# Kernel optimization log

Measured on AMD Instinct MI355X. Metric: run time of the kernel, lower is better.

## Reference

```python
import jax, jax.numpy as jnp
import numpy as np

N_NODES = 100000
N_EDGES = 1600000
IN_FEATS = 256
OUT_FEATS = 128


def setup_inputs() -> dict:
    key = jax.random.key(0)
    k1, k2, k3, k4 = jax.random.split(key, 4)
    feat = jax.random.normal(k1, (N_NODES, IN_FEATS), dtype=jnp.float32)
    W = jax.random.normal(k2, (IN_FEATS, OUT_FEATS), dtype=jnp.float32)
    src = jax.random.randint(k3, (N_EDGES,), 0, N_NODES, dtype=jnp.int64)
    dst = jax.random.randint(k4, (N_EDGES,), 0, N_NODES, dtype=jnp.int64)
    return {"feat": feat, "W": W, "src": src, "dst": dst}


def reference(feat, W, src, dst):
    # h_self = feat @ W  -> [N, out_feats]
    h_self = feat @ W
    # update_all(copy_src('h','m'), sum('m','neigh')): gather source features,
    # scatter-sum at destination nodes (SpMM over the edge list).
    msgs = h_self[src]                                        # [E, out_feats]
    h_neigh = jax.ops.segment_sum(msgs, dst, num_segments=N_NODES)
    # in-degree per node
    degs = jax.ops.segment_sum(jnp.ones(dst.shape, jnp.float32), dst,
                               num_segments=N_NODES)          # [N]
    rst = (h_neigh + h_self) / (degs[:, None] + 1.0)
    return jax.nn.relu(rst)
```

## Files before the change

kernel.cpp:

```cpp
#include <hip/hip_runtime.h>
#include <hip/hip_bf16.h>


#define IN_FEATS 256
#define OUT_FEATS 128
#define NUM_NODES 100000
#define NUM_EDGES 1600000

#define NB 782
#define EC 128
#define CHUNK_E 12500
#define BCAP 3072
#define GEMM_BLOCKS 391

typedef __attribute__((ext_vector_type(8))) short short8;
typedef __attribute__((ext_vector_type(8))) unsigned short ushort8;
typedef __attribute__((ext_vector_type(4))) float f32x4;

static __device__ inline unsigned short f2bfu(float x) {
    union { __hip_bfloat16 h; unsigned short u; } c;
    c.h = __float2bfloat16(x);
    return c.u;
}
static __device__ inline ushort2 f2bfu2(float x, float y) {
    union { __hip_bfloat162 h; ushort2 u; } c;
    c.h = __float22bfloat162_rn(make_float2(x, y));
    return c.u;
}
static __device__ inline float bf2f(unsigned short h) {
    return __uint_as_float((unsigned)h << 16);
}

__global__ __launch_bounds__(256) void convert_hist(
    const float* __restrict__ W, unsigned short* __restrict__ Wt,
    const int* __restrict__ dst, int* __restrict__ counts)
{
    int b = blockIdx.x;
    int t = threadIdx.x;
    if (b < 128) {
        int i = b * 256 + t;
        int n = i >> 8;
        int k = i & 255;
        Wt[i] = f2bfu(W[(size_t)k * OUT_FEATS + n]);
        return;
    }
    int c = b - 128;
    __shared__ int hist[NB];
    for (int i = t; i < NB; i += 256) hist[i] = 0;
    __syncthreads();
    const int4* dp = (const int4*)(dst + c * CHUNK_E);
    for (int i = t; i < CHUNK_E / 4; i += 256) {
        int4 d4 = dp[i];
        atomicAdd(&hist[d4.x >> 7], 1);
        atomicAdd(&hist[d4.y >> 7], 1);
        atomicAdd(&hist[d4.z >> 7], 1);
        atomicAdd(&hist[d4.w >> 7], 1);
    }
    __syncthreads();
    for (int i = t; i < NB; i += 256) counts[c * NB + i] = hist[i];
}

__global__ __launch_bounds__(128) void scan_chunks(
    int* __restrict__ counts, int* __restrict__ bucket_total)
{
    __shared__ int sd[128];
    int b = blockIdx.x, t = threadIdx.x;
    int v = counts[t * NB + b];
    sd[t] = v;
    __syncthreads();
    for (int o = 1; o < 128; o <<= 1) {
        int x = (t >= o) ? sd[t - o] : 0;
        __syncthreads();
        sd[t] += x;
        __syncthreads();
    }
    counts[t * NB + b] = sd[t] - v;
    if (t == 127) bucket_total[b] = sd[127];
}

__global__ __launch_bounds__(256) void scan_buckets(
    const int* __restrict__ bucket_total, int* __restrict__ bucket_base)
{
    __shared__ int sd[256];
    int t = threadIdx.x;
    int base = t * 4;
    int v0 = 0, v1 = 0, v2 = 0, v3 = 0;
    if (base + 3 < NB) {
        int4 v = *(const int4*)&bucket_total[base];
        v0 = v.x; v1 = v.y; v2 = v.z; v3 = v.w;
    } else {
        if (base + 0 < NB) v0 = bucket_total[base + 0];
        if (base + 1 < NB) v1 = bucket_total[base + 1];
        if (base + 2 < NB) v2 = bucket_total[base + 2];
        if (base + 3 < NB) v3 = bucket_total[base + 3];
    }
    int s = v0 + v1 + v2 + v3;
    sd[t] = s;
    __syncthreads();
    for (int o = 1; o < 256; o <<= 1) {
        int x = (t >= o) ? sd[t - o] : 0;
        __syncthreads();
        sd[t] += x;
        __syncthreads();
    }
    int e0 = sd[t] - s, e1 = e0 + v0, e2 = e1 + v1, e3 = e2 + v2;
    if (base + 0 < NB) bucket_base[base + 0] = e0;
    if (base + 1 < NB) bucket_base[base + 1] = e1;
    if (base + 2 < NB) bucket_base[base + 2] = e2;
    if (base + 3 < NB) bucket_base[base + 3] = e3;
}

__global__ __launch_bounds__(512) void scatter_k(
    const int* __restrict__ src, const int* __restrict__ dst,
    const int* __restrict__ counts, const int* __restrict__ bucket_base,
    int* __restrict__ bedges)
{
    __shared__ int cur[NB];
    const int tid = threadIdx.x;
    int c = blockIdx.x;
    for (int i = tid; i < NB; i += 512)
        cur[i] = bucket_base[i] + counts[c * NB + i];
    __syncthreads();
    const int4* dp = (const int4*)(dst + c * CHUNK_E);
    const int4* sp = (const int4*)(src + c * CHUNK_E);
    for (int i = tid; i < CHUNK_E / 4; i += 512) {
        int4 d4 = dp[i];
        int4 s4 = sp[i];
        int dv[4] = { d4.x, d4.y, d4.z, d4.w };
        int sv[4] = { s4.x, s4.y, s4.z, s4.w };
#pragma unroll
        for (int j = 0; j < 4; ++j) {
            int d = dv[j];
            int slot = atomicAdd(&cur[d >> 7], 1);
            bedges[slot] = sv[j] | ((d & 127) << 17);
        }
    }
}

static __device__ inline void stage_chunk(
    const float* __restrict__ feat, char* smem, int buf,
    int bm0, int k0, int t, int M)
{
#pragma unroll
    for (int j = 0; j < 4; ++j) {
        int G = j * 512 + t;
        int r = G >> 3;
        int g = G & 7;
        int srow = bm0 + r;
        if (srow > M - 1) srow = M - 1;
        const float* src = feat + (size_t)srow * IN_FEATS + k0 + ((g ^ (r & 7)) << 2);
        __builtin_amdgcn_global_load_lds(
            (const __attribute__((address_space(1))) unsigned int*)src,
            (__attribute__((address_space(3))) unsigned int*)(smem + buf * 32768 + G * 16),
            16, 0, 0);
    }
}

__global__ __launch_bounds__(512, 4) void gemm_k(
    const float* __restrict__ feat, const unsigned short* __restrict__ Wt,
    unsigned short* __restrict__ hself16, int M)
{
    __shared__ char smem_raw[65536];
    const int tid = threadIdx.x;

    const int w  = tid >> 6;
    const int l  = tid & 63;
    const int lf = l & 15;
    const int lg = (l >> 4) & 3;
    const int bm0 = blockIdx.x * 256;

    f32x4 acc[2][8];
#pragma unroll
    for (int mt = 0; mt < 2; ++mt)
#pragma unroll
        for (int nt = 0; nt < 8; ++nt)
            acc[mt][nt] = (f32x4){0.f, 0.f, 0.f, 0.f};

    stage_chunk(feat, smem_raw, 0, bm0, 0, tid, M);
    __syncthreads();

#pragma unroll
    for (int kc = 0; kc < 8; ++kc) {
        const int buf = kc & 1;
        if (kc < 7)
            stage_chunk(feat, smem_raw, buf ^ 1, bm0, (kc + 1) * 32, tid, M);

        const int k8 = kc * 4;

        short8 af[2];
#pragma unroll
        for (int mt = 0; mt < 2; ++mt) {
            int r  = w * 32 + mt * 16 + lf;
            int rs = r & 7;
            const char* base = smem_raw + buf * 32768 + r * 128;
            float4 f0 = *(const float4*)(base + ((((lg << 1) + 0) ^ rs) << 4));
            float4 f1 = *(const float4*)(base + ((((lg << 1) + 1) ^ rs) << 4));
            ushort2 c0 = f2bfu2(f0.x, f0.y);
            ushort2 c1 = f2bfu2(f0.z, f0.w);
            ushort2 c2 = f2bfu2(f1.x, f1.y);
            ushort2 c3 = f2bfu2(f1.z, f1.w);
            af[mt] = (short8){ (short)c0.x, (short)c0.y, (short)c1.x, (short)c1.y,
                               (short)c2.x, (short)c2.y, (short)c3.x, (short)c3.y };
        }

#pragma unroll
        for (int nh = 0; nh < 2; ++nh) {
            short8 bf[4];
#pragma unroll
            for (int q = 0; q < 4; ++q) {
                int nt = nh * 4 + q;
                int n = nt * 16 + lf;
                bf[q] = *(const short8*)(Wt + (size_t)n * IN_FEATS + (k8 + lg) * 8);
            }
#pragma unroll
            for (int q = 0; q < 4; ++q) {
                int nt = nh * 4 + q;
                acc[0][nt] = __builtin_amdgcn_mfma_f32_16x16x32_bf16(af[0], bf[q], acc[0][nt], 0, 0, 0);
                acc[1][nt] = __builtin_amdgcn_mfma_f32_16x16x32_bf16(af[1], bf[q], acc[1][nt], 0, 0, 0);
            }
        }

        __syncthreads();
    }

    unsigned short* ep = (unsigned short*)smem_raw;
#pragma unroll
    for (int mt = 0; mt < 2; ++mt)
#pragma unroll
        for (int nt = 0; nt < 8; ++nt)
#pragma unroll
            for (int r = 0; r < 4; ++r) {
                int row = w * 32 + mt * 16 + lg * 4 + r;
                ep[row * 128 + nt * 16 + lf] = f2bfu(acc[mt][nt][r]);
            }
    __syncthreads();
#pragma unroll
    for (int i = 0; i < 8; ++i) {
        int lrow = w * 32 + i * 4 + (l >> 4);
        ushort8 v = *(const ushort8*)(ep + lrow * 128 + (l & 15) * 8);
        int grow = bm0 + lrow;
        if (grow < M)
            *(ushort8*)(hself16 + (size_t)grow * OUT_FEATS + (l & 15) * 8) = v;
    }
}

__global__ __launch_bounds__(512, 8) void sort_gather(
    const int* __restrict__ bucket_base, const int* __restrict__ bucket_total,
    const int* __restrict__ bedges, const unsigned short* __restrict__ hself16,
    float* __restrict__ out)
{
    __shared__ int sorted[BCAP];
    __shared__ int cnt[128], off[128], cursor[128], sd[128];

    int b = blockIdx.x, t = threadIdx.x;
    int base = bucket_base[b];
    int tot = bucket_total[b];
    if (tot > BCAP) tot = BCAP;
    int nnodes = NUM_NODES - b * 128;
    if (nnodes > 128) nnodes = 128;

    if (t < 128) cnt[t] = 0;
    __syncthreads();
    for (int i = t; i < tot; i += 512)
        atomicAdd(&cnt[bedges[base + i] >> 17], 1);
    __syncthreads();
    if (t < 128) sd[t] = cnt[t];
    __syncthreads();
    for (int o = 1; o < 128; o <<= 1) {
        int x = 0;
        if (t < 128 && t >= o) x = sd[t - o];
        __syncthreads();
        if (t < 128) sd[t] += x;
        __syncthreads();
    }
    if (t < 128) { int e = sd[t] - cnt[t]; off[t] = e; cursor[t] = e; }
    __syncthreads();
    for (int i = t; i < tot; i += 512) {
        int e = bedges[base + i];
        int r = atomicAdd(&cursor[e >> 17], 1);
        sorted[r] = e & 0x1FFFF;
    }
    __syncthreads();

    int w = t >> 6, l = t & 63, lg = l >> 4, lf = l & 15;
    for (int ln = w; ln < nnodes; ln += 8) {
        int beg = off[ln];
        int end = beg + cnt[ln];
        float acc[8];
#pragma unroll
        for (int i = 0; i < 8; ++i) acc[i] = 0.f;
        for (int j0 = beg; j0 < end; j0 += 16) {
            int  jj[4];
            bool pp[4];
            int  ss[4];
#pragma unroll
            for (int q = 0; q < 4; ++q) {
                jj[q] = j0 + q * 4 + lg;
                pp[q] = jj[q] < end;
                ss[q] = pp[q] ? sorted[jj[q]] : 0;
            }
            ushort8 h[4];
#pragma unroll
            for (int q = 0; q < 4; ++q)
                h[q] = *(const ushort8*)(hself16 + (size_t)ss[q] * OUT_FEATS + lf * 8);
#pragma unroll
            for (int q = 0; q < 4; ++q)
                if (pp[q]) {
#pragma unroll
                    for (int i = 0; i < 8; ++i) acc[i] += bf2f(h[q][i]);
                }
        }
#pragma unroll
        for (int i = 0; i < 8; ++i) {
            acc[i] += __shfl_xor(acc[i], 16, 64);
            acc[i] += __shfl_xor(acc[i], 32, 64);
        }
        if (lg == 0) {
            int n = b * 128 + ln;
            float inv = 1.0f / (float)(end - beg + 1);
            ushort8 hs = *(const ushort8*)(hself16 + (size_t)n * OUT_FEATS + lf * 8);
            float v[8];
#pragma unroll
            for (int i = 0; i < 8; ++i)
                v[i] = fmaxf((acc[i] + bf2f(hs[i])) * inv, 0.f);
            float4* op = (float4*)(out + (size_t)n * OUT_FEATS + lf * 8);
            op[0] = make_float4(v[0], v[1], v[2], v[3]);
            op[1] = make_float4(v[4], v[5], v[6], v[7]);
        }
    }
}

extern "C" void kernel_launch(void* const* d_in, const int* in_sizes, int n_in,
                              void* d_out, int out_size, void* d_ws, size_t ws_size,
                              hipStream_t stream) {
    const float* feat = (const float*)d_in[0];
    const float* W    = (const float*)d_in[1];
    const int*   src  = (const int*)d_in[2];
    const int*   dst  = (const int*)d_in[3];
    float* out = (float*)d_out;

    char* ws = (char*)d_ws;
    unsigned short* hself16 = (unsigned short*)ws;
    unsigned short* Wt      = (unsigned short*)(ws + 25600000);
    int* counts       = (int*)(ws + 25665536);
    int* bucket_total = (int*)(ws + 26065920);
    int* bucket_base  = (int*)(ws + 26069120);
    int* bedges       = (int*)(ws + 26072320);

    convert_hist<<<256, 256, 0, stream>>>(W, Wt, dst, counts);
    scan_chunks<<<NB, 128, 0, stream>>>(counts, bucket_total);
    scan_buckets<<<1, 256, 0, stream>>>(bucket_total, bucket_base);
    scatter_k<<<EC, 512, 0, stream>>>(src, dst, counts, bucket_base, bedges);
    gemm_k<<<GEMM_BLOCKS, 512, 0, stream>>>(feat, Wt, hself16, NUM_NODES);
    sort_gather<<<NB, 512, 0, stream>>>(bucket_base, bucket_total, bedges, hself16, out);
}
```

Measured before the change: 292.8 us.

## Split sort and gather kernels; assign one 16-lane group per node

The fused sort+gather kernel is split into a sort kernel and a gather kernel. The sort kernel writes the per-bucket sorted source indices back to global memory and stores a packed offset/count per node. The gather kernel assigns one 16-lane group to each node, with 8 outstanding row loads per iteration, which removes the cross-lane shuffle reduction and lets the self-row load be issued early. This frees the gather from shared-memory sort overhead and allows lower occupancy bounds, at the cost of an extra launch and an extra round trip of the edge array through global memory.

Result: no change. 297.2 us (+1.5%).

```diff
diff --git a/kernel.cpp b/kernel.cpp
--- a/kernel.cpp
+++ b/kernel.cpp
@@ -244,14 +244,52 @@
     }
 }
 
-__global__ __launch_bounds__(512, 8) void sort_gather(
+__global__ __launch_bounds__(512, 8) void sort_k(
     const int* __restrict__ bucket_base, const int* __restrict__ bucket_total,
-    const int* __restrict__ bedges, const unsigned short* __restrict__ hself16,
-    float* __restrict__ out)
+    int* __restrict__ bedges, int* __restrict__ nodeinfo)
 {
     __shared__ int sorted[BCAP];
     __shared__ int cnt[128], off[128], cursor[128], sd[128];
 
+    int b = blockIdx.x, t = threadIdx.x;
+    int base = bucket_base[b];
+    int tot = bucket_total[b];
+    if (tot > BCAP) tot = BCAP;
+
+    if (t < 128) cnt[t] = 0;
+    __syncthreads();
+    for (int i = t; i < tot; i += 512)
+        atomicAdd(&cnt[bedges[base + i] >> 17], 1);
+    __syncthreads();
+    if (t < 128) sd[t] = cnt[t];
+    __syncthreads();
+    for (int o = 1; o < 128; o <<= 1) {
+        int x = 0;
+        if (t < 128 && t >= o) x = sd[t - o];
+        __syncthreads();
+        if (t < 128) sd[t] += x;
+        __syncthreads();
+    }
+    if (t < 128) { int e = sd[t] - cnt[t]; off[t] = e; cursor[t] = e; }
+    __syncthreads();
+    for (int i = t; i < tot; i += 512) {
+        int e = bedges[base + i];
+        int r = atomicAdd(&cursor[e >> 17], 1);
+        sorted[r] = e & 0x1FFFF;
+    }
+    __syncthreads();
+    for (int i = t; i < tot; i += 512)
+        bedges[base + i] = sorted[i];
+    if (t < 128)
+        nodeinfo[b * 128 + t] = (off[t] << 16) | cnt[t];
+}
+
+__global__ __launch_bounds__(512, 4) void gather_k(
+    const int* __restrict__ bucket_base, const int* __restrict__ bucket_total,
+    const int* __restrict__ bedges, const int* __restrict__ nodeinfo,
+    const unsigned short* __restrict__ hself16, float* __restrict__ out)
+{
+    __shared__ int sorted[BCAP];
     int b = blockIdx.x, t = threadIdx.x;
     int base = bucket_base[b];
     int tot = bucket_total[b];
@@ -259,74 +297,57 @@
     int nnodes = NUM_NODES - b * 128;
     if (nnodes > 128) nnodes = 128;
 
-    if (t < 128) cnt[t] = 0;
-    __syncthreads();
     for (int i = t; i < tot; i += 512)
-        atomicAdd(&cnt[bedges[base + i] >> 17], 1);
-    __syncthreads();
-    if (t < 128) sd[t] = cnt[t];
-    __syncthreads();
-    for (int o = 1; o < 128; o <<= 1) {
-        int x = 0;
-        if (t < 128 && t >= o) x = sd[t - o];
-        __syncthreads();
-        if (t < 128) sd[t] += x;
-        __syncthreads();
-    }
-    if (t < 128) { int e = sd[t] - cnt[t]; off[t] = e; cursor[t] = e; }
-    __syncthreads();
-    for (int i = t; i < tot; i += 512) {
-        int e = bedges[base + i];
-        int r = atomicAdd(&cursor[e >> 17], 1);
-        sorted[r] = e & 0x1FFFF;
-    }
-    __syncthreads();
-
-    int w = t >> 6, l = t & 63, lg = l >> 4, lf = l & 15;
-    for (int ln = w; ln < nnodes; ln += 8) {
-        int beg = off[ln];
-        int end = beg + cnt[ln];
+        sorted[i] = bedges[base + i];
+    __syncthreads();
+
+    const int gid = t >> 4;
+    const int lf  = t & 15;
+
+#pragma unroll
+    for (int rep = 0; rep < 4; ++rep) {
+        int ln = rep * 32 + gid;
+        if (ln >= nnodes) continue;
+        int info = nodeinfo[b * 128 + ln];
+        int beg = info >> 16;
+        int cn  = info & 0xFFFF;
+        int end = beg + cn;
+        int n = b * 128 + ln;
+        ushort8 hs = *(const ushort8*)(hself16 + (size_t)n * OUT_FEATS + lf * 8);
+
         float acc[8];
 #pragma unroll
         for (int i = 0; i < 8; ++i) acc[i] = 0.f;
-        for (int j0 = beg; j0 < end; j0 += 16) {
-            int  jj[4];
-            bool pp[4];
-            int  ss[4];
-#pragma unroll
-            for (int q = 0; q < 4; ++q) {
-                jj[q] = j0 + q * 4 + lg;
-                pp[q] = jj[q] < end;
-                ss[q] = pp[q] ? sorted[jj[q]] : 0;
+
+        for (int j0 = beg; j0 < end; j0 += 8) {
+            int  ss[8];
+            bool pp[8];
+#pragma unroll
+            for (int q = 0; q < 8; ++q) {
+                int jj = j0 + q;
+                pp[q] = jj < end;
+                ss[q] = pp[q] ? sorted[jj] : 0;
             }
-            ushort8 h[4];
-#pragma unroll
-            for (int q = 0; q < 4; ++q)
+            ushort8 h[8];
+#pragma unroll
+            for (int q = 0; q < 8; ++q)
                 h[q] = *(const ushort8*)(hself16 + (size_t)ss[q] * OUT_FEATS + lf * 8);
 #pragma unroll
-            for (int q = 0; q < 4; ++q)
+            for (int q = 0; q < 8; ++q)
                 if (pp[q]) {
 #pragma unroll
                     for (int i = 0; i < 8; ++i) acc[i] += bf2f(h[q][i]);
                 }
         }
-#pragma unroll
-        for (int i = 0; i < 8; ++i) {
-            acc[i] += __shfl_xor(acc[i], 16, 64);
-            acc[i] += __shfl_xor(acc[i], 32, 64);
-        }
-        if (lg == 0) {
-            int n = b * 128 + ln;
-            float inv = 1.0f / (float)(end - beg + 1);
-            ushort8 hs = *(const ushort8*)(hself16 + (size_t)n * OUT_FEATS + lf * 8);
-            float v[8];
-#pragma unroll
-            for (int i = 0; i < 8; ++i)
-                v[i] = fmaxf((acc[i] + bf2f(hs[i])) * inv, 0.f);
-            float4* op = (float4*)(out + (size_t)n * OUT_FEATS + lf * 8);
-            op[0] = make_float4(v[0], v[1], v[2], v[3]);
-            op[1] = make_float4(v[4], v[5], v[6], v[7]);
-        }
+
+        float inv = 1.0f / (float)(cn + 1);
+        float v[8];
+#pragma unroll
+        for (int i = 0; i < 8; ++i)
+            v[i] = fmaxf((acc[i] + bf2f(hs[i])) * inv, 0.f);
+        float4* op = (float4*)(out + (size_t)n * OUT_FEATS + lf * 8);
+        op[0] = make_float4(v[0], v[1], v[2], v[3]);
+        op[1] = make_float4(v[4], v[5], v[6], v[7]);
     }
 }
 
@@ -346,11 +367,14 @@
     int* bucket_total = (int*)(ws + 26065920);
     int* bucket_base  = (int*)(ws + 26069120);
     int* bedges       = (int*)(ws + 26072320);
+    int* nodeinfo     = counts;
 
     convert_hist<<<256, 256, 0, stream>>>(W, Wt, dst, counts);
     scan_chunks<<<NB, 128, 0, stream>>>(counts, bucket_total);
     scan_buckets<<<1, 256, 0, stream>>>(bucket_total, bucket_base);
     scatter_k<<<EC, 512, 0, stream>>>(src, dst, counts, bucket_base, bedges);
     gemm_k<<<GEMM_BLOCKS, 512, 0, stream>>>(feat, Wt, hself16, NUM_NODES);
-    sort_gather<<<NB, 512, 0, stream>>>(bucket_base, bucket_total, bedges, hself16, out);
-}
+    sort_k<<<NB, 512, 0, stream>>>(bucket_base, bucket_total, bedges, nodeinfo);
+    gather_k<<<NB, 512, 0, stream>>>(bucket_base, bucket_total, bedges, nodeinfo,
+                                     hself16, out);
+}
```
